# Kernel optimization log

Hardware: AMD Instinct MI355X
Metric: run time of the kernel (lower is better)

Reference implementation:

```python
import jax, jax.numpy as jnp
import numpy as np

L = 18                      # tree depth, N = 2**L - 1 nodes (complete binary tree)
N = 2**L - 1               # 262143
D = 128                     # embedding dim
V = 100000                  # vocab size of the single data type
E = 8                       # edge_count


def setup_inputs() -> dict:
    key = jax.random.key(0)
    ks = jax.random.split(key, 8)
    data = jax.random.randint(ks[0], (N,), 0, V)
    edges = jax.random.randint(ks[1], (N,), 0, E)
    data_vecs = jax.random.normal(ks[2], (V, D), dtype=jnp.float32) * 0.1
    # torch uses torch.rand (U[0,1)); scaled for numerical stability over 18 levels
    data_W = jax.random.uniform(ks[3], (D, D), dtype=jnp.float32) * 0.1
    data_b = jax.random.uniform(ks[4], (D,), dtype=jnp.float32) * 0.1
    edge_W = jax.random.uniform(ks[5], (E, D, D), dtype=jnp.float32) * (2.0 / D)
    edge_b = jax.random.uniform(ks[6], (E, D), dtype=jnp.float32) * 0.1
    score_W = jax.random.uniform(ks[7], (D, 1), dtype=jnp.float32)
    return {"data": data, "edges": edges, "data_vecs": data_vecs,
            "data_W": data_W, "data_b": data_b, "edge_W": edge_W,
            "edge_b": edge_b, "score_W": score_W}


def reference(data, edges, data_vecs, data_W, data_b, edge_W, edge_b, score_W):
    # per-node leaf term: addmm(data_bias, data_vecs[data], data_W)  -> [N, D]
    raw = data_vecs[data] @ data_W + data_b
    ret = raw    # value returned to the parent (leaves: unclamped)
    emb = raw    # stored embedding (internal nodes: pre-clamp h)
    # bottom-up over levels; level l occupies indices [2**l - 1, 2**(l+1) - 1)
    for l in reversed(range(L - 1)):
        p0, npar = 2**l - 1, 2**l
        c0, M = 2**(l + 1) - 1, 2**(l + 1)
        child_ret = ret[c0:c0 + M]              # [M, D], siblings adjacent
        eids = edges[c0:c0 + M]                 # [M]
        # edge-weighted child transform: child @ edge_W[e] + edge_b[e]
        contrib = edge_b[eids]
        for e in range(E):                      # small static edge loop
            contrib = contrib + jnp.where((eids == e)[:, None], child_ret, 0.0) @ edge_W[e]
        # sum the two children of each parent, then (leaf + children) / (nc + 1)
        contrib = contrib.reshape(npar, 2, D).sum(axis=1)
        h = (raw[p0:p0 + npar] + contrib) / 3.0
        emb = emb.at[p0:p0 + npar].set(h)
        ret = ret.at[p0:p0 + npar].set(jnp.maximum(h, 0.0))
    scores = (emb @ score_W)[:, 0]              # [N]
    return scores


if __name__ == "__main__":
    out = reference(**setup_inputs())
    print(out.shape, out.dtype)
```

## Files before the change

kernel.cpp:

```cpp
#include <hip/hip_runtime.h>

#define D 128
#define TS 64
#define LDSTR 136
#define CHUNK 2048
#define PLVL0 10
#define CBASE 2047
#define NBINS 56
#define NRAW 2047
#define PLACE_BLKS 127
#define LEAF_CAP 17408
#define LEAF_TILES 2176
#define PERM_TOTAL 286208

typedef float  floatx4 __attribute__((ext_vector_type(4)));
typedef short  shortx8 __attribute__((ext_vector_type(8)));

__device__ __constant__ int d_pcap[7]  = {384, 704, 1280, 2432, 4608, 8960, 17408};
__device__ __constant__ int d_pbase[7] = {0, 3072, 8704, 18944, 38400, 75264, 146944};

__device__ __forceinline__ unsigned short f2bf(float f) {
    unsigned u = __float_as_uint(f);
    u += 0x7FFFu + ((u >> 16) & 1u);
    return (unsigned short)(u >> 16);
}
__device__ __forceinline__ float bf2f(unsigned short h) {
    return __uint_as_float(((unsigned)h) << 16);
}

__global__ __launch_bounds__(256) void prep_kernel(
    const float* __restrict__ dW, const float* __restrict__ db,
    const float* __restrict__ eW, const float* __restrict__ eb,
    const float* __restrict__ sWs, const float* __restrict__ vecs,
    const int* __restrict__ edges,
    unsigned short* __restrict__ ewt, unsigned short* __restrict__ cwt,
    unsigned short* __restrict__ dwt, float* __restrict__ dcomp,
    float* __restrict__ sv, float* __restrict__ s0, int* __restrict__ ctr,
    int* __restrict__ perm, int Nn,
    unsigned short* __restrict__ vbf, int n4)
{
    __shared__ float smem[8448];
    const int b = blockIdx.x, t = threadIdx.x;
    if (b < 32) {
        float* w_s = smem;
        float* cs  = smem + 4096;
        const int e = b >> 2, cc = b & 3;
        for (int i = t; i < D * 8; i += 256) {
            const int k = i >> 3, j4 = i & 7;
            ((float4*)w_s)[i] = ((const float4*)eW)[((size_t)e * D + k) * 32 + cc * 8 + j4];
        }
        __syncthreads();
        const int r2 = t >> 1, h = t & 1;
        float4 acc[4];
        #pragma unroll
        for (int m = 0; m < 4; m++) acc[m] = make_float4(0.f, 0.f, 0.f, 0.f);
        for (int k = 0; k < D; k++) {
            const float a = dW[(size_t)r2 * D + k];
            #pragma unroll
            for (int m = 0; m < 4; m++) {
                const float4 w4 = ((const float4*)w_s)[k * 8 + h * 4 + m];
                acc[m].x += a * w4.x; acc[m].y += a * w4.y; acc[m].z += a * w4.z; acc[m].w += a * w4.w;
            }
        }
        #pragma unroll
        for (int m = 0; m < 4; m++) {
            cs[r2 * 33 + h * 16 + m * 4 + 0] = acc[m].x;
            cs[r2 * 33 + h * 16 + m * 4 + 1] = acc[m].y;
            cs[r2 * 33 + h * 16 + m * 4 + 2] = acc[m].z;
            cs[r2 * 33 + h * 16 + m * 4 + 3] = acc[m].w;
        }
        __syncthreads();
        {
            const int nn = t >> 3, kseg = t & 7, k0 = kseg * 16;
            unsigned ow[8];
            #pragma unroll
            for (int i2 = 0; i2 < 8; i2++) {
                const unsigned short lo = f2bf(cs[(k0 + 2 * i2) * 33 + nn]);
                const unsigned short hi = f2bf(cs[(k0 + 2 * i2 + 1) * 33 + nn]);
                ow[i2] = (unsigned)lo | ((unsigned)hi << 16);
            }
            uint4* dstp = (uint4*)(cwt + (size_t)e * D * D + (size_t)(cc * 32 + nn) * D + k0);
            dstp[0] = make_uint4(ow[0], ow[1], ow[2], ow[3]);
            dstp[1] = make_uint4(ow[4], ow[5], ow[6], ow[7]);
        }
        if (t < 32) {
            float a2 = 0.f;
            for (int k = 0; k < D; k++) a2 += db[k] * w_s[k * 32 + t];
            dcomp[e * D + cc * 32 + t] = a2 + eb[e * D + cc * 32 + t];
        }
    } else if (b < 41) {
        float* lds = smem;
        const int bb = b - 32;
        const float* src = (bb < 8) ? (eW + (size_t)bb * D * D) : dW;
        unsigned short* dst = (bb < 8) ? (ewt + (size_t)bb * D * D) : dwt;
        for (int half = 0; half < 2; half++) {
            __syncthreads();
            for (int i = t; i < 64 * D / 4; i += 256) {
                float4 v = ((const float4*)src)[half * (64 * D / 4) + i];
                const int k = (i * 4) >> 7, n = (i * 4) & 127;
                lds[k * 129 + n]     = v.x;
                lds[k * 129 + n + 1] = v.y;
                lds[k * 129 + n + 2] = v.z;
                lds[k * 129 + n + 3] = v.w;
            }
            __syncthreads();
            const int n = t >> 1, hh = t & 1;
            for (int kk = 0; kk < 32; kk++) {
                const int k = hh * 32 + kk;
                dst[(size_t)n * D + half * 64 + k] = f2bf(lds[k * 129 + n]);
            }
        }
    } else if (b == 41) {
        float* red = smem;
        if (t < D) {
            float acc = 0.f;
            for (int j = 0; j < D; j++) acc += dW[(size_t)t * D + j] * sWs[j];
            sv[t] = acc;
        }
        red[t] = (t < D) ? db[t] * sWs[t] : 0.f;
        __syncthreads();
        for (int s = 128; s > 0; s >>= 1) { if (t < s) red[t] += red[t + s]; __syncthreads(); }
        if (t == 0) s0[0] = red[0];
    } else if (b < 42 + PLACE_BLKS) {
        unsigned char* key_s = (unsigned char*)smem;
        int* lcnt  = (int*)(smem + 512);
        int* lbase = (int*)(smem + 576);
        if (t < NBINS) lcnt[t] = 0;
        __syncthreads();
        const int base = CBASE + (b - 42) * CHUNK;
        for (int i = t; i < CHUNK; i += 256) {
            const int c = base + i;
            if (c < Nn) {
                const int e = edges[c];
                const int p = (c - 1) >> 1;
                const int l = 31 - __clz(p + 1);
                const int kk = (l - PLVL0) * 8 + e;
                key_s[i] = (unsigned char)kk;
                atomicAdd(&lcnt[kk], 1);
            } else key_s[i] = 255;
        }
        __syncthreads();
        if (t < NBINS) {
            const int n = lcnt[t];
            lbase[t] = n ? atomicAdd(&ctr[t], n) : 0;
            lcnt[t] = 0;
        }
        __syncthreads();
        for (int i = t; i < CHUNK; i += 256) {
            const int c = base + i;
            if (c >= Nn) continue;
            const int kk = key_s[i];
            if (kk == 255) continue;
            const int off = atomicAdd(&lcnt[kk], 1);
            const int li = kk >> 3, e = kk & 7;
            const int pos = lbase[kk] + off;
            if (pos < d_pcap[li])
                perm[d_pbase[li] + e * d_pcap[li] + pos] = c;
        }
    } else {
        for (int i = (b - 42 - PLACE_BLKS) * 256 + t; i < n4; i += (gridDim.x - 42 - PLACE_BLKS) * 256) {
            const float4 v = ((const float4*)vecs)[i];
            uint2 o;
            o.x = (unsigned)f2bf(v.x) | ((unsigned)f2bf(v.y) << 16);
            o.y = (unsigned)f2bf(v.z) | ((unsigned)f2bf(v.w) << 16);
            ((uint2*)vbf)[i] = o;
        }
    }
}

__global__ __launch_bounds__(256, 6) void leaf_embed_kernel(
    unsigned short* __restrict__ X,
    const unsigned short* __restrict__ vbf,
    const int* __restrict__ data,
    const int* __restrict__ perm,
    const int* __restrict__ cnt8,
    const unsigned short* __restrict__ cwt,
    const float* __restrict__ dcomp,
    const float* __restrict__ sv, const float* __restrict__ s0p,
    const unsigned short* __restrict__ dwt,
    const float* __restrict__ db,
    float* __restrict__ out,
    int lbase_leaf)
{
    __shared__ unsigned short a_s[TS * LDSTR];
    const int t = threadIdx.x;
    const bool is_leaf = (blockIdx.x < LEAF_TILES);
    const int r = t >> 2, h4 = t & 3;

    int c;
    const unsigned short* Wg;
    const float* bias;
    if (is_leaf) {
        const int ts = blockIdx.x * TS;
        const int e = ts / LEAF_CAP;
        const int rb = ts - e * LEAF_CAP;
        const int fill = min(cnt8[e], LEAF_CAP);
        if (rb >= fill) return;
        c = (rb + r < fill) ? perm[lbase_leaf + e * LEAF_CAP + rb + r] : -1;
        Wg = cwt + (size_t)e * D * D;
        bias = dcomp + (size_t)e * D;
    } else {
        const int node = (blockIdx.x - LEAF_TILES) * TS + r;
        c = (node < NRAW) ? node : -1;
        Wg = dwt;
        bias = db;
    }

    {
        unsigned short* dst = a_s + r * LDSTR + h4 * 32;
        if (c >= 0) {
            const uint4* src = (const uint4*)(vbf + (size_t)data[c] * D + h4 * 32);
            if (is_leaf) {
                float sc = 0.f;
                #pragma unroll
                for (int j = 0; j < 4; j++) {
                    const uint4 v = src[j];
                    const unsigned* pv = (const unsigned*)&v;
                    #pragma unroll
                    for (int u = 0; u < 4; u++) {
                        const int n = h4 * 32 + j * 8 + u * 2;
                        sc += bf2f((unsigned short)pv[u]) * sv[n]
                            + bf2f((unsigned short)(pv[u] >> 16)) * sv[n + 1];
                    }
                    ((uint4*)dst)[j] = v;
                }
                sc += __shfl_xor(sc, 1, 64);
                sc += __shfl_xor(sc, 2, 64);
                if (h4 == 0) out[c] = sc + s0p[0];
            } else {
                #pragma unroll
                for (int j = 0; j < 4; j++) ((uint4*)dst)[j] = src[j];
            }
        } else {
            #pragma unroll
            for (int j = 0; j < 4; j++) ((uint4*)dst)[j] = make_uint4(0u, 0u, 0u, 0u);
        }
    }
    __syncthreads();

    const int lane = t & 63, wv = t >> 6;
    const int cq = lane & 15, q = lane >> 4;
    const floatx4 z4 = {0.f, 0.f, 0.f, 0.f};
    floatx4 acc[4][2];
    #pragma unroll
    for (int i = 0; i < 4; i++) { acc[i][0] = z4; acc[i][1] = z4; }
    #pragma unroll
    for (int ks = 0; ks < 4; ks++) {
        shortx8 bfr[2];
        #pragma unroll
        for (int nl = 0; nl < 2; nl++) {
            const int n = (wv * 2 + nl) * 16 + cq;
            bfr[nl] = *(const shortx8*)(Wg + (size_t)n * D + ks * 32 + q * 8);
        }
        #pragma unroll
        for (int mt = 0; mt < 4; mt++) {
            const shortx8 af = *(const shortx8*)(a_s + (mt * 16 + cq) * LDSTR + ks * 32 + q * 8);
            acc[mt][0] = __builtin_amdgcn_mfma_f32_16x16x32_bf16(bfr[0], af, acc[mt][0], 0, 0, 0);
            acc[mt][1] = __builtin_amdgcn_mfma_f32_16x16x32_bf16(bfr[1], af, acc[mt][1], 0, 0, 0);
        }
    }
    __syncthreads();
    #pragma unroll
    for (int nl = 0; nl < 2; nl++) {
        const int n0 = (wv * 2 + nl) * 16 + q * 4;
        const float4 b4 = *(const float4*)(bias + n0);
        #pragma unroll
        for (int mt = 0; mt < 4; mt++) {
            const int m = mt * 16 + cq;
            const unsigned lo = (unsigned)f2bf(acc[mt][nl][0] + b4.x)
                              | ((unsigned)f2bf(acc[mt][nl][1] + b4.y) << 16);
            const unsigned hi = (unsigned)f2bf(acc[mt][nl][2] + b4.z)
                              | ((unsigned)f2bf(acc[mt][nl][3] + b4.w) << 16);
            *(uint2*)(a_s + (size_t)m * LDSTR + n0) = make_uint2(lo, hi);
        }
    }
    __syncthreads();
    if (c >= 0) {
        uint4* dstg = (uint4*)(X + (size_t)c * D + h4 * 32);
        const uint4* srcl = (const uint4*)(a_s + r * LDSTR + h4 * 32);
        #pragma unroll
        for (int j = 0; j < 4; j++) dstg[j] = srcl[j];
    }
}

__global__ __launch_bounds__(256, 3) void tree_fused_kernel(
    unsigned short* __restrict__ X,
    const unsigned short* __restrict__ vbf,
    const int* __restrict__ data,
    const int* __restrict__ perm,
    const int* __restrict__ cnt8,
    int Cl, int lbase,
    const unsigned short* __restrict__ dwt,
    const float* __restrict__ db,
    const unsigned short* __restrict__ ewt,
    const float* __restrict__ eb,
    const float* __restrict__ svec,
    float* __restrict__ out)
{
    __shared__ unsigned short a_s[TS * LDSTR];
    __shared__ float cs_s[TS][132];
    __shared__ float scorebuf[TS];
    const int t = threadIdx.x;
    const int ts = blockIdx.x * TS;
    const int e = ts / Cl;
    const int rb = ts - e * Cl;
    const int fill = min(cnt8[e], Cl);
    if (rb >= fill) return;
    const int r = t >> 2, h4 = t & 3;
    const int c = (rb + r < fill) ? perm[lbase + e * Cl + rb + r] : -1;

    if (t < TS) scorebuf[t] = 0.f;
    {
        unsigned short* dst = a_s + r * LDSTR + h4 * 32;
        float* cd = &cs_s[r][h4 * 32];
        if (c >= 0) {
            const uint4* src = (const uint4*)(vbf + (size_t)data[c] * D + h4 * 32);
            const uint4* ya = (const uint4*)(X + (size_t)(2 * c + 1) * D + h4 * 32);
            const uint4* yb = (const uint4*)(X + (size_t)(2 * c + 2) * D + h4 * 32);
            #pragma unroll
            for (int j = 0; j < 4; j++) {
                ((uint4*)dst)[j] = src[j];
                const uint4 rbv = ya[j], rcv = yb[j];
                const unsigned* pb = (const unsigned*)&rbv;
                const unsigned* pc = (const unsigned*)&rcv;
                #pragma unroll
                for (int u = 0; u < 4; u++) {
                    cd[j * 8 + u * 2]     = bf2f((unsigned short)pb[u]) + bf2f((unsigned short)pc[u]);
                    cd[j * 8 + u * 2 + 1] = bf2f((unsigned short)(pb[u] >> 16)) + bf2f((unsigned short)(pc[u] >> 16));
                }
            }
        } else {
            #pragma unroll
            for (int j = 0; j < 4; j++) {
                ((uint4*)dst)[j] = make_uint4(0u, 0u, 0u, 0u);
                ((float4*)cd)[j * 2]     = make_float4(0.f, 0.f, 0.f, 0.f);
                ((float4*)cd)[j * 2 + 1] = make_float4(0.f, 0.f, 0.f, 0.f);
            }
        }
    }
    __syncthreads();

    const int lane = t & 63, wv = t >> 6;
    const int cq = lane & 15, q = lane >> 4;
    const floatx4 z4 = {0.f, 0.f, 0.f, 0.f};
    floatx4 acc[4][2];
    #pragma unroll
    for (int i = 0; i < 4; i++) { acc[i][0] = z4; acc[i][1] = z4; }
    #pragma unroll
    for (int ks = 0; ks < 4; ks++) {
        shortx8 bfr[2];
        #pragma unroll
        for (int nl = 0; nl < 2; nl++) {
            const int n = (wv * 2 + nl) * 16 + cq;
            bfr[nl] = *(const shortx8*)(dwt + (size_t)n * D + ks * 32 + q * 8);
        }
        #pragma unroll
        for (int mt = 0; mt < 4; mt++) {
            const shortx8 af = *(const shortx8*)(a_s + (mt * 16 + cq) * LDSTR + ks * 32 + q * 8);
            acc[mt][0] = __builtin_amdgcn_mfma_f32_16x16x32_bf16(bfr[0], af, acc[mt][0], 0, 0, 0);
            acc[mt][1] = __builtin_amdgcn_mfma_f32_16x16x32_bf16(bfr[1], af, acc[mt][1], 0, 0, 0);
        }
    }
    const float inv3 = 1.0f / 3.0f;
    float sp[4] = {0.f, 0.f, 0.f, 0.f};
    uint2 hpk[2][4];
    #pragma unroll
    for (int nl = 0; nl < 2; nl++) {
        const int n0 = (wv * 2 + nl) * 16 + q * 4;
        const float4 db4 = *(const float4*)(db + n0);
        const float4 sv4 = *(const float4*)(svec + n0);
        #pragma unroll
        for (int mt = 0; mt < 4; mt++) {
            const int m = mt * 16 + cq;
            const float4 cs4 = *(const float4*)(&cs_s[m][n0]);
            const float h0 = (acc[mt][nl][0] + db4.x + cs4.x) * inv3;
            const float h1 = (acc[mt][nl][1] + db4.y + cs4.y) * inv3;
            const float h2 = (acc[mt][nl][2] + db4.z + cs4.z) * inv3;
            const float h3 = (acc[mt][nl][3] + db4.w + cs4.w) * inv3;
            sp[mt] += h0 * sv4.x + h1 * sv4.y + h2 * sv4.z + h3 * sv4.w;
            unsigned short q0 = f2bf(h0), q1 = f2bf(h1), q2 = f2bf(h2), q3 = f2bf(h3);
            q0 = (q0 & 0x8000u) ? 0 : q0;
            q1 = (q1 & 0x8000u) ? 0 : q1;
            q2 = (q2 & 0x8000u) ? 0 : q2;
            q3 = (q3 & 0x8000u) ? 0 : q3;
            hpk[nl][mt] = make_uint2((unsigned)q0 | ((unsigned)q1 << 16),
                                     (unsigned)q2 | ((unsigned)q3 << 16));
        }
    }
    #pragma unroll
    for (int mt = 0; mt < 4; mt++) {
        sp[mt] += __shfl_xor(sp[mt], 16, 64);
        sp[mt] += __shfl_xor(sp[mt], 32, 64);
    }
    __syncthreads();
    #pragma unroll
    for (int nl = 0; nl < 2; nl++) {
        const int n0 = (wv * 2 + nl) * 16 + q * 4;
        #pragma unroll
        for (int mt = 0; mt < 4; mt++)
            *(uint2*)(a_s + (size_t)(mt * 16 + cq) * LDSTR + n0) = hpk[nl][mt];
    }
    if (q == 0) {
        #pragma unroll
        for (int mt = 0; mt < 4; mt++) atomicAdd(&scorebuf[mt * 16 + cq], sp[mt]);
    }
    __syncthreads();
    const unsigned short* Wg = ewt + (size_t)e * D * D;
    #pragma unroll
    for (int i = 0; i < 4; i++) { acc[i][0] = z4; acc[i][1] = z4; }
    #pragma unroll
    for (int ks = 0; ks < 4; ks++) {
        shortx8 bfr[2];
        #pragma unroll
        for (int nl = 0; nl < 2; nl++) {
            const int n = (wv * 2 + nl) * 16 + cq;
            bfr[nl] = *(const shortx8*)(Wg + (size_t)n * D + ks * 32 + q * 8);
        }
        #pragma unroll
        for (int mt = 0; mt < 4; mt++) {
            const shortx8 af = *(const shortx8*)(a_s + (mt * 16 + cq) * LDSTR + ks * 32 + q * 8);
            acc[mt][0] = __builtin_amdgcn_mfma_f32_16x16x32_bf16(bfr[0], af, acc[mt][0], 0, 0, 0);
            acc[mt][1] = __builtin_amdgcn_mfma_f32_16x16x32_bf16(bfr[1], af, acc[mt][1], 0, 0, 0);
        }
    }
    __syncthreads();
    #pragma unroll
    for (int nl = 0; nl < 2; nl++) {
        const int n0 = (wv * 2 + nl) * 16 + q * 4;
        const float4 b4 = *(const float4*)(eb + (size_t)e * D + n0);
        #pragma unroll
        for (int mt = 0; mt < 4; mt++) {
            const int m = mt * 16 + cq;
            const unsigned lo = (unsigned)f2bf(acc[mt][nl][0] + b4.x)
                              | ((unsigned)f2bf(acc[mt][nl][1] + b4.y) << 16);
            const unsigned hi = (unsigned)f2bf(acc[mt][nl][2] + b4.z)
                              | ((unsigned)f2bf(acc[mt][nl][3] + b4.w) << 16);
            *(uint2*)(a_s + (size_t)m * LDSTR + n0) = make_uint2(lo, hi);
        }
    }
    __syncthreads();
    if (c >= 0) {
        uint4* dstg = (uint4*)(X + (size_t)c * D + h4 * 32);
        const uint4* srcl = (const uint4*)(a_s + r * LDSTR + h4 * 32);
        #pragma unroll
        for (int j = 0; j < 4; j++) dstg[j] = srcl[j];
        if (h4 == 1) out[c] = scorebuf[r];
    }
}

__global__ __launch_bounds__(256) void sub_kernel(
    unsigned short* __restrict__ X,
    const float* __restrict__ eW,
    const float* __restrict__ eb,
    const int* __restrict__ edges,
    const float* __restrict__ sW,
    float* __restrict__ out,
    int rbase, int nlev)
{
    __shared__ __align__(16) float xbuf[4][D];
    const int t = threadIdx.x, wv = t >> 6, lane = t & 63;
    const int u = rbase + blockIdx.x;
    const int j2 = lane * 2;
    const float inv3 = 1.0f / 3.0f;

    for (int lev = nlev - 1; lev >= 0; lev--) {
        const int first = ((u + 1) << lev) - 1;
        const int cnt = 1 << lev;
        for (int i = wv; i < cnt; i += 4) {
            const int n = first + i;
            const unsigned ra = *(const unsigned*)(X + (size_t)n * D + j2);
            const unsigned rb = *(const unsigned*)(X + (size_t)(2 * n + 1) * D + j2);
            const unsigned rc = *(const unsigned*)(X + (size_t)(2 * n + 2) * D + j2);
            const float h0 = (bf2f((unsigned short)ra) + bf2f((unsigned short)rb)
                            + bf2f((unsigned short)rc)) * inv3;
            const float h1 = (bf2f((unsigned short)(ra >> 16)) + bf2f((unsigned short)(rb >> 16))
                            + bf2f((unsigned short)(rc >> 16))) * inv3;
            float sc = h0 * sW[j2] + h1 * sW[j2 + 1];
            #pragma unroll
            for (int o = 32; o > 0; o >>= 1) sc += __shfl_xor(sc, o, 64);
            if (lane == 0) out[n] = sc;
            if (n == 0) continue;
            float2 x2 = make_float2(fmaxf(h0, 0.f), fmaxf(h1, 0.f));
            *(float2*)(xbuf[wv] + j2) = x2;
            const int e = edges[n];
            const float* W = eW + (size_t)e * D * D;
            float y0 = 0.f, y1 = 0.f;
            #pragma unroll 8
            for (int k4 = 0; k4 < 32; k4++) {
                const float4 xk = *(const float4*)(xbuf[wv] + k4 * 4);
                const float2 w0 = *(const float2*)(W + (size_t)(k4 * 4 + 0) * D + j2);
                const float2 w1 = *(const float2*)(W + (size_t)(k4 * 4 + 1) * D + j2);
                const float2 w2 = *(const float2*)(W + (size_t)(k4 * 4 + 2) * D + j2);
                const float2 w3 = *(const float2*)(W + (size_t)(k4 * 4 + 3) * D + j2);
                y0 += xk.x * w0.x + xk.y * w1.x + xk.z * w2.x + xk.w * w3.x;
                y1 += xk.x * w0.y + xk.y * w1.y + xk.z * w2.y + xk.w * w3.y;
            }
            y0 += eb[e * D + j2];
            y1 += eb[e * D + j2 + 1];
            const unsigned o = (unsigned)f2bf(y0) | ((unsigned)f2bf(y1) << 16);
            *(unsigned*)(X + (size_t)n * D + j2) = o;
        }
        __syncthreads();
    }
}

extern "C" void kernel_launch(void* const* d_in, const int* in_sizes, int n_in,
                              void* d_out, int out_size, void* d_ws, size_t ws_size,
                              hipStream_t stream) {
    const int*   data      = (const int*)d_in[0];
    const int*   edges     = (const int*)d_in[1];
    const float* data_vecs = (const float*)d_in[2];
    const float* data_W    = (const float*)d_in[3];
    const float* data_b    = (const float*)d_in[4];
    const float* edge_W    = (const float*)d_in[5];
    const float* edge_b    = (const float*)d_in[6];
    const float* score_W   = (const float*)d_in[7];
    float* out = (float*)d_out;

    const int Nn = in_sizes[0];
    const int VD = in_sizes[2];

    static const int caps[7]  = {384, 704, 1280, 2432, 4608, 8960, 17408};
    static const int bases[7] = {0, 3072, 8704, 18944, 38400, 75264, 146944};

    char* w = (char*)d_ws;
    size_t off = 0;
    unsigned short* X = (unsigned short*)(w + off); off += (size_t)Nn * D * 2;
    int* perm = (int*)(w + off);  off += (size_t)PERM_TOTAL * 4;
    off = (off + 255) & ~(size_t)255;
    int* ctr     = (int*)(w + off); off += 64 * 4;
    off = (off + 255) & ~(size_t)255;
    float* dcomp = (float*)(w + off); off += 8 * D * 4;
    float* sv    = (float*)(w + off); off += D * 4;
    float* s0    = (float*)(w + off); off += 256;
    off = (off + 255) & ~(size_t)255;
    unsigned short* ewt = (unsigned short*)(w + off); off += (size_t)8 * D * D * 2;
    unsigned short* cwt = (unsigned short*)(w + off); off += (size_t)8 * D * D * 2;
    unsigned short* dwt = (unsigned short*)(w + off); off += (size_t)D * D * 2;
    off = (off + 255) & ~(size_t)255;
    unsigned short* vbf = (unsigned short*)(w + off); off += (size_t)VD * 2;

    hipMemsetAsync(ctr, 0, 64 * 4, stream);

    prep_kernel<<<42 + PLACE_BLKS + 1024, 256, 0, stream>>>(
        data_W, data_b, edge_W, edge_b, score_W, data_vecs, edges,
        ewt, cwt, dwt, dcomp, sv, s0, ctr, perm, Nn, vbf, VD / 4);

    leaf_embed_kernel<<<LEAF_TILES + (NRAW + TS - 1) / TS, 256, 0, stream>>>(
        X, vbf, data, perm, ctr + 48,
        cwt, dcomp, sv, s0, dwt, data_b, out, bases[6]);

    for (int l = 15; l >= PLVL0; l--) {
        const int li = l - PLVL0;
        const int grid = caps[li] * 8 / TS;
        tree_fused_kernel<<<grid, 256, 0, stream>>>(
            X, vbf, data, perm, ctr + li * 8, caps[li], bases[li],
            dwt, data_b, ewt, edge_b, score_W, out);
    }

    sub_kernel<<<128, 256, 0, stream>>>(X, edge_W, edge_b, edges, score_W, out, 127, 4);
    sub_kernel<<<8, 256, 0, stream>>>(X, edge_W, edge_b, edges, score_W, out, 7, 4);
    sub_kernel<<<1, 256, 0, stream>>>(X, edge_W, edge_b, edges, score_W, out, 0, 3);
}
```

Measured before the change: 274.2 us.

## Bucket tree nodes per chunk locally instead of global per-level edge bins

```diff
diff --git a/kernel.cpp b/kernel.cpp
--- a/kernel.cpp
+++ b/kernel.cpp
@@ -6,18 +6,17 @@
 #define CHUNK 2048
 #define PLVL0 10
 #define CBASE 2047
-#define NBINS 56
 #define NRAW 2047
-#define PLACE_BLKS 127
-#define LEAF_CAP 17408
-#define LEAF_TILES 2176
-#define PERM_TOTAL 286208
+#define NCHUNKS 127
+#define ECAP 384
+#define CHUNK_STRIDE (8*ECAP)
+#define SLOTS 6
+#define TILES_PER_CHUNK 48
+#define LEAF_CHUNK0 63
+#define LEAF_TILES 3072
 
 typedef float  floatx4 __attribute__((ext_vector_type(4)));
 typedef short  shortx8 __attribute__((ext_vector_type(8)));
-
-__device__ __constant__ int d_pcap[7]  = {384, 704, 1280, 2432, 4608, 8960, 17408};
-__device__ __constant__ int d_pbase[7] = {0, 3072, 8704, 18944, 38400, 75264, 146944};
 
 __device__ __forceinline__ unsigned short f2bf(float f) {
     unsigned u = __float_as_uint(f);
@@ -35,8 +34,8 @@
     const int* __restrict__ edges,
     unsigned short* __restrict__ ewt, unsigned short* __restrict__ cwt,
     unsigned short* __restrict__ dwt, float* __restrict__ dcomp,
-    float* __restrict__ sv, float* __restrict__ s0, int* __restrict__ ctr,
-    int* __restrict__ perm, int Nn,
+    float* __restrict__ sv, float* __restrict__ s0,
+    int* __restrict__ gcnt, int* __restrict__ perm,
     unsigned short* __restrict__ vbf, int n4)
 {
     __shared__ float smem[8448];
@@ -121,44 +120,23 @@
         __syncthreads();
         for (int s = 128; s > 0; s >>= 1) { if (t < s) red[t] += red[t + s]; __syncthreads(); }
         if (t == 0) s0[0] = red[0];
-    } else if (b < 42 + PLACE_BLKS) {
-        unsigned char* key_s = (unsigned char*)smem;
-        int* lcnt  = (int*)(smem + 512);
-        int* lbase = (int*)(smem + 576);
-        if (t < NBINS) lcnt[t] = 0;
+    } else if (b < 42 + NCHUNKS) {
+        int* lcnt = (int*)smem;
+        if (t < 8) lcnt[t] = 0;
         __syncthreads();
-        const int base = CBASE + (b - 42) * CHUNK;
+        const int chunk = b - 42;
+        const int base = CBASE + chunk * CHUNK;
         for (int i = t; i < CHUNK; i += 256) {
             const int c = base + i;
-            if (c < Nn) {
-                const int e = edges[c];
-                const int p = (c - 1) >> 1;
-                const int l = 31 - __clz(p + 1);
-                const int kk = (l - PLVL0) * 8 + e;
-                key_s[i] = (unsigned char)kk;
-                atomicAdd(&lcnt[kk], 1);
-            } else key_s[i] = 255;
+            const int e = edges[c];
+            const int off = atomicAdd(&lcnt[e], 1);
+            if (off < ECAP)
+                perm[(size_t)chunk * CHUNK_STRIDE + e * ECAP + off] = c;
         }
         __syncthreads();
-        if (t < NBINS) {
-            const int n = lcnt[t];
-            lbase[t] = n ? atomicAdd(&ctr[t], n) : 0;
-            lcnt[t] = 0;
-        }
-        __syncthreads();
-        for (int i = t; i < CHUNK; i += 256) {
-            const int c = base + i;
-            if (c >= Nn) continue;
-            const int kk = key_s[i];
-            if (kk == 255) continue;
-            const int off = atomicAdd(&lcnt[kk], 1);
-            const int li = kk >> 3, e = kk & 7;
-            const int pos = lbase[kk] + off;
-            if (pos < d_pcap[li])
-                perm[d_pbase[li] + e * d_pcap[li] + pos] = c;
-        }
+        if (t < 8) gcnt[chunk * 8 + t] = lcnt[t];
     } else {
-        for (int i = (b - 42 - PLACE_BLKS) * 256 + t; i < n4; i += (gridDim.x - 42 - PLACE_BLKS) * 256) {
+        for (int i = (b - 42 - NCHUNKS) * 256 + t; i < n4; i += (gridDim.x - 42 - NCHUNKS) * 256) {
             const float4 v = ((const float4*)vecs)[i];
             uint2 o;
             o.x = (unsigned)f2bf(v.x) | ((unsigned)f2bf(v.y) << 16);
@@ -173,14 +151,13 @@
     const unsigned short* __restrict__ vbf,
     const int* __restrict__ data,
     const int* __restrict__ perm,
-    const int* __restrict__ cnt8,
+    const int* __restrict__ gcnt,
     const unsigned short* __restrict__ cwt,
     const float* __restrict__ dcomp,
     const float* __restrict__ sv, const float* __restrict__ s0p,
     const unsigned short* __restrict__ dwt,
     const float* __restrict__ db,
-    float* __restrict__ out,
-    int lbase_leaf)
+    float* __restrict__ out)
 {
     __shared__ unsigned short a_s[TS * LDSTR];
     const int t = threadIdx.x;
@@ -191,12 +168,14 @@
     const unsigned short* Wg;
     const float* bias;
     if (is_leaf) {
-        const int ts = blockIdx.x * TS;
-        const int e = ts / LEAF_CAP;
-        const int rb = ts - e * LEAF_CAP;
-        const int fill = min(cnt8[e], LEAF_CAP);
+        const int crel = blockIdx.x / TILES_PER_CHUNK;
+        const int rem  = blockIdx.x % TILES_PER_CHUNK;
+        const int e = rem / SLOTS, slot = rem % SLOTS;
+        const int chunk = LEAF_CHUNK0 + crel;
+        const int fill = min(gcnt[chunk * 8 + e], ECAP);
+        const int rb = slot * TS;
         if (rb >= fill) return;
-        c = (rb + r < fill) ? perm[lbase_leaf + e * LEAF_CAP + rb + r] : -1;
+        c = (rb + r < fill) ? perm[(size_t)chunk * CHUNK_STRIDE + e * ECAP + rb + r] : -1;
         Wg = cwt + (size_t)e * D * D;
         bias = dcomp + (size_t)e * D;
     } else {
@@ -288,8 +267,8 @@
     const unsigned short* __restrict__ vbf,
     const int* __restrict__ data,
     const int* __restrict__ perm,
-    const int* __restrict__ cnt8,
-    int Cl, int lbase,
+    const int* __restrict__ gcnt,
+    int chunk0,
     const unsigned short* __restrict__ dwt,
     const float* __restrict__ db,
     const unsigned short* __restrict__ ewt,
@@ -301,13 +280,15 @@
     __shared__ float cs_s[TS][132];
     __shared__ float scorebuf[TS];
     const int t = threadIdx.x;
-    const int ts = blockIdx.x * TS;
-    const int e = ts / Cl;
-    const int rb = ts - e * Cl;
-    const int fill = min(cnt8[e], Cl);
+    const int crel = blockIdx.x / TILES_PER_CHUNK;
+    const int rem  = blockIdx.x % TILES_PER_CHUNK;
+    const int e = rem / SLOTS, slot = rem % SLOTS;
+    const int chunk = chunk0 + crel;
+    const int fill = min(gcnt[chunk * 8 + e], ECAP);
+    const int rb = slot * TS;
     if (rb >= fill) return;
     const int r = t >> 2, h4 = t & 3;
-    const int c = (rb + r < fill) ? perm[lbase + e * Cl + rb + r] : -1;
+    const int c = (rb + r < fill) ? perm[(size_t)chunk * CHUNK_STRIDE + e * ECAP + rb + r] : -1;
 
     if (t < TS) scorebuf[t] = 0.f;
     {
@@ -520,15 +501,12 @@
     const int Nn = in_sizes[0];
     const int VD = in_sizes[2];
 
-    static const int caps[7]  = {384, 704, 1280, 2432, 4608, 8960, 17408};
-    static const int bases[7] = {0, 3072, 8704, 18944, 38400, 75264, 146944};
-
     char* w = (char*)d_ws;
     size_t off = 0;
     unsigned short* X = (unsigned short*)(w + off); off += (size_t)Nn * D * 2;
-    int* perm = (int*)(w + off);  off += (size_t)PERM_TOTAL * 4;
+    int* perm = (int*)(w + off);  off += (size_t)NCHUNKS * CHUNK_STRIDE * 4;
     off = (off + 255) & ~(size_t)255;
-    int* ctr     = (int*)(w + off); off += 64 * 4;
+    int* gcnt    = (int*)(w + off); off += NCHUNKS * 8 * 4;
     off = (off + 255) & ~(size_t)255;
     float* dcomp = (float*)(w + off); off += 8 * D * 4;
     float* sv    = (float*)(w + off); off += D * 4;
@@ -540,21 +518,18 @@
     off = (off + 255) & ~(size_t)255;
     unsigned short* vbf = (unsigned short*)(w + off); off += (size_t)VD * 2;
 
-    hipMemsetAsync(ctr, 0, 64 * 4, stream);
-
-    prep_kernel<<<42 + PLACE_BLKS + 1024, 256, 0, stream>>>(
+    prep_kernel<<<42 + NCHUNKS + 1024, 256, 0, stream>>>(
         data_W, data_b, edge_W, edge_b, score_W, data_vecs, edges,
-        ewt, cwt, dwt, dcomp, sv, s0, ctr, perm, Nn, vbf, VD / 4);
+        ewt, cwt, dwt, dcomp, sv, s0, gcnt, perm, vbf, VD / 4);
 
     leaf_embed_kernel<<<LEAF_TILES + (NRAW + TS - 1) / TS, 256, 0, stream>>>(
-        X, vbf, data, perm, ctr + 48,
-        cwt, dcomp, sv, s0, dwt, data_b, out, bases[6]);
+        X, vbf, data, perm, gcnt, cwt, dcomp, sv, s0, dwt, data_b, out);
 
     for (int l = 15; l >= PLVL0; l--) {
-        const int li = l - PLVL0;
-        const int grid = caps[li] * 8 / TS;
-        tree_fused_kernel<<<grid, 256, 0, stream>>>(
-            X, vbf, data, perm, ctr + li * 8, caps[li], bases[li],
+        const int nch = 1 << (l - PLVL0);
+        const int chunk0 = nch - 1;
+        tree_fused_kernel<<<nch * TILES_PER_CHUNK, 256, 0, stream>>>(
+            X, vbf, data, perm, gcnt, chunk0,
             dwt, data_b, ewt, edge_b, score_W, out);
     }
 
```

Result: no change. 273.9 us (median of 2 runs) (-0.1%).
